# Performance work log

Measured on AMD Instinct MI355X. Metric: run time of the kernel, lower is better.

The kernel has to match this reference:

```python
import jax, jax.numpy as jnp
import numpy as np

HIDDEN = 2048
INTER = 8192
COMPRESSION = 128.9

def _n_ctrl(out_size, in_size):
    return max(16, int(out_size * in_size / COMPRESSION))

def _catmull_rom_grid(n_ctrl, n_samples):
    # static (numpy, float64) sampling grid over [0, n_ctrl-1] to avoid fp32 precision loss
    t = np.linspace(0.0, n_ctrl - 1.0, n_samples, dtype=np.float64)
    i = np.clip(np.floor(t).astype(np.int64), 0, n_ctrl - 2)
    f = (t - i).astype(np.float32)
    idx = np.stack([np.clip(i + k, 0, n_ctrl - 1) for k in (-1, 0, 1, 2)], axis=0)  # [4, N]
    return jnp.asarray(idx.astype(np.int32)), jnp.asarray(f)

def spline_reconstruct(control_points, out_size, in_size):
    """Cubic (Catmull-Rom, order-3) interpolation of 1D control points to a dense [out,in] weight."""
    n = out_size * in_size
    idx, f = _catmull_rom_grid(control_points.shape[0], n)
    p0, p1, p2, p3 = control_points[idx[0]], control_points[idx[1]], control_points[idx[2]], control_points[idx[3]]
    f2 = f * f
    f3 = f2 * f
    w = 0.5 * (2.0 * p1 + (p2 - p0) * f
               + (2.0 * p0 - 5.0 * p1 + 4.0 * p2 - p3) * f2
               + (3.0 * p1 - p0 - 3.0 * p2 + p3) * f3)
    return w.reshape(out_size, in_size)

def setup_inputs() -> dict:
    key = jax.random.key(0)
    k0, k1, k2, k3 = jax.random.split(key, 4)
    hidden_states = jax.random.normal(k0, (4, 2048, HIDDEN), dtype=jnp.float32)
    gate_cp = jax.random.normal(k1, (_n_ctrl(INTER, HIDDEN),), dtype=jnp.float32) * 0.02
    up_cp = jax.random.normal(k2, (_n_ctrl(INTER, HIDDEN),), dtype=jnp.float32) * 0.02
    down_cp = jax.random.normal(k3, (_n_ctrl(HIDDEN, INTER),), dtype=jnp.float32) * 0.02
    return {"hidden_states": hidden_states, "gate_cp": gate_cp, "up_cp": up_cp, "down_cp": down_cp}

def reference(hidden_states, gate_cp, up_cp, down_cp):
    gate_w = spline_reconstruct(gate_cp, INTER, HIDDEN)   # [I, H]
    up_w = spline_reconstruct(up_cp, INTER, HIDDEN)       # [I, H]
    down_w = spline_reconstruct(down_cp, HIDDEN, INTER)   # [H, I]
    gate = jnp.einsum('bsh,ih->bsi', hidden_states, gate_w)
    up = jnp.einsum('bsh,ih->bsi', hidden_states, up_w)
    inter = jax.nn.silu(gate) * up
    return jnp.einsum('bsi,hi->bsh', inter, down_w)
```

## Files before the change

### kernel.cpp

```cpp
#include <hip/hip_runtime.h>
#include <hip/hip_bf16.h>
#include <math.h>

using bf16 = __hip_bfloat16;
typedef __bf16 bf16x8 __attribute__((ext_vector_type(8)));
typedef float  f32x4  __attribute__((ext_vector_type(4)));

#define BK 64

__global__ void spline_recon8_kernel(const float* __restrict__ cp,
                                     bf16* __restrict__ w,
                                     int n8, int n_ctrl, double step) {
    int k8 = blockIdx.x * blockDim.x + threadIdx.x;
    if (k8 >= n8) return;
    long long kbase = (long long)k8 * 8;
    bf16x8 o;
#pragma unroll
    for (int u = 0; u < 8; ++u) {
        double t = (double)(kbase + u) * step;
        int i = (int)t;
        if (i > n_ctrl - 2) i = n_ctrl - 2;
        float f = (float)(t - (double)i);
        float p0 = cp[i > 0 ? i - 1 : 0];
        float p1 = cp[i];
        float p2 = cp[i + 1];
        float p3 = cp[(i + 2) <= (n_ctrl - 1) ? (i + 2) : (n_ctrl - 1)];
        float f2 = f * f;
        float f3 = f2 * f;
        float v = 0.5f * (2.0f * p1
                          + (p2 - p0) * f
                          + (2.0f * p0 - 5.0f * p1 + 4.0f * p2 - p3) * f2
                          + (3.0f * p1 - p0 - 3.0f * p2 + p3) * f3);
        o[u] = (__bf16)v;
    }
    *reinterpret_cast<bf16x8*>(w + kbase) = o;
}

__global__ void cvt_f32_bf16_8_kernel(const float4* __restrict__ x,
                                      bf16* __restrict__ y, int n8) {
    int k = blockIdx.x * blockDim.x + threadIdx.x;
    if (k >= n8) return;
    float4 a = x[2 * k];
    float4 b = x[2 * k + 1];
    bf16x8 o;
    o[0] = (__bf16)a.x; o[1] = (__bf16)a.y; o[2] = (__bf16)a.z; o[3] = (__bf16)a.w;
    o[4] = (__bf16)b.x; o[5] = (__bf16)b.y; o[6] = (__bf16)b.z; o[7] = (__bf16)b.w;
    *reinterpret_cast<bf16x8*>(y + (long long)k * 8) = o;
}

__device__ __forceinline__ void async_load16(const bf16* g, bf16* l) {
    __builtin_amdgcn_global_load_lds(
        (const __attribute__((address_space(1))) void*)g,
        (__attribute__((address_space(3))) void*)l,
        16, 0, 0);
}

__global__ __launch_bounds__(512, 4) void fused_gate_up_kernel(
    const bf16* __restrict__ A,
    const bf16* __restrict__ Bg,
    const bf16* __restrict__ Bu,
    bf16* __restrict__ C,
    int M, int N, int K) {
    __shared__ __align__(16) bf16 smem[3 * 128 * BK];
    bf16* As  = smem;
    bf16* Bgs = smem + 128 * BK;
    bf16* Bus = smem + 2 * 128 * BK;

    const int tid  = threadIdx.x;
    const int lane = tid & 63;
    const int wave = tid >> 6;
    const int wq   = wave & 3;
    const int wm   = (wq >> 1) * 64;
    const int wn   = (wq & 1) * 64;
    const bool is_gate = wave < 4;

    const long long brow = (long long)blockIdx.y * 128;
    const long long bcol = (long long)blockIdx.x * 128;

    const int srow = tid >> 3;
    const int skb  = ((tid & 7) ^ (srow & 7)) * 8;
    const bf16* ga0 = A  + (brow + srow) * (long long)K + skb;
    const bf16* ga1 = A  + (brow + srow + 64) * (long long)K + skb;
    const bf16* gg0 = Bg + (bcol + srow) * (long long)K + skb;
    const bf16* gg1 = Bg + (bcol + srow + 64) * (long long)K + skb;
    const bf16* gu0 = Bu + (bcol + srow) * (long long)K + skb;
    const bf16* gu1 = Bu + (bcol + srow + 64) * (long long)K + skb;
    bf16* la0 = As  + tid * 8;
    bf16* la1 = As  + 4096 + tid * 8;
    bf16* lg0 = Bgs + tid * 8;
    bf16* lg1 = Bgs + 4096 + tid * 8;
    bf16* lu0 = Bus + tid * 8;
    bf16* lu1 = Bus + 4096 + tid * 8;

    const bf16* Bsel = is_gate ? Bgs : Bus;
    const int fm = wm + (lane & 15);
    const int fn = wn + (lane & 15);
    const int qk = lane >> 4;

    f32x4 acc[4][4] = {};

    for (int k0 = 0; k0 < K; k0 += BK) {
        async_load16(ga0, la0); ga0 += BK;
        async_load16(ga1, la1); ga1 += BK;
        async_load16(gg0, lg0); gg0 += BK;
        async_load16(gg1, lg1); gg1 += BK;
        async_load16(gu0, lu0); gu0 += BK;
        async_load16(gu1, lu1); gu1 += BK;
        __syncthreads();

#pragma unroll
        for (int h = 0; h < 2; ++h) {
            bf16x8 afr[4], bfr[4];
            const int hc = (h << 2) | qk;
            const int ccA = (hc ^ (fm & 7)) * 8;
            const int ccB = (hc ^ (fn & 7)) * 8;
#pragma unroll
            for (int i = 0; i < 4; ++i)
                afr[i] = *reinterpret_cast<const bf16x8*>(
                    &As[(fm + i * 16) * BK + ccA]);
#pragma unroll
            for (int j = 0; j < 4; ++j)
                bfr[j] = *reinterpret_cast<const bf16x8*>(
                    &Bsel[(fn + j * 16) * BK + ccB]);
#pragma unroll
            for (int i = 0; i < 4; ++i)
#pragma unroll
                for (int j = 0; j < 4; ++j)
                    acc[i][j] = __builtin_amdgcn_mfma_f32_16x16x32_bf16(
                        afr[i], bfr[j], acc[i][j], 0, 0, 0);
        }
        __syncthreads();
    }

    bf16* Epi = smem;
    if (is_gate) {
#pragma unroll
        for (int i = 0; i < 4; ++i)
#pragma unroll
            for (int j = 0; j < 4; ++j)
#pragma unroll
                for (int r = 0; r < 4; ++r) {
                    int row = wm + i * 16 + (lane >> 4) * 4 + r;
                    int col = wn + j * 16 + (lane & 15);
                    float v = acc[i][j][r];
                    float s = v / (1.0f + expf(-v));
                    Epi[row * 128 + col] = __float2bfloat16(s);
                }
    }
    __syncthreads();
    if (!is_gate) {
#pragma unroll
        for (int i = 0; i < 4; ++i)
#pragma unroll
            for (int j = 0; j < 4; ++j)
#pragma unroll
                for (int r = 0; r < 4; ++r) {
                    int row = wm + i * 16 + (lane >> 4) * 4 + r;
                    int col = wn + j * 16 + (lane & 15);
                    float s = __bfloat162float(Epi[row * 128 + col]);
                    float v = s * acc[i][j][r];
                    C[(brow + row) * (long long)N + bcol + col] = __float2bfloat16(v);
                }
    }
}

__global__ __launch_bounds__(256, 4) void gemm_down3_kernel(
    const bf16* __restrict__ A,
    const bf16* __restrict__ B,
    float* __restrict__ C,
    int M, int N, int K) {
    __shared__ __align__(16) bf16 As[128 * BK];
    __shared__ __align__(16) bf16 Bs[128 * BK];

    const int tid  = threadIdx.x;
    const int lane = tid & 63;
    const int wave = tid >> 6;
    const int wm   = (wave >> 1) * 64;
    const int wn   = (wave & 1) * 64;

    const long long brow = (long long)blockIdx.y * 128;
    const long long bcol = (long long)blockIdx.x * 128;

    const int srow = tid >> 3;
    const int skb  = ((tid & 7) ^ (srow & 7)) * 8;
    const bf16* ga = A + (brow + srow) * (long long)K + skb;
    const bf16* gb = B + (bcol + srow) * (long long)K + skb;
    const long long rstep = 32LL * K;

    const int fm = wm + (lane & 15);
    const int fn = wn + (lane & 15);
    const int qk = lane >> 4;

    f32x4 acc[4][4] = {};

    for (int k0 = 0; k0 < K; k0 += BK) {
#pragma unroll
        for (int r = 0; r < 4; ++r) {
            async_load16(ga + r * rstep, As + r * 2048 + tid * 8);
            async_load16(gb + r * rstep, Bs + r * 2048 + tid * 8);
        }
        ga += BK; gb += BK;
        __syncthreads();

#pragma unroll
        for (int h = 0; h < 2; ++h) {
            bf16x8 afr[4], bfr[4];
            const int hc = (h << 2) | qk;
            const int ccA = (hc ^ (fm & 7)) * 8;
            const int ccB = (hc ^ (fn & 7)) * 8;
#pragma unroll
            for (int i = 0; i < 4; ++i)
                afr[i] = *reinterpret_cast<const bf16x8*>(
                    &As[(fm + i * 16) * BK + ccA]);
#pragma unroll
            for (int j = 0; j < 4; ++j)
                bfr[j] = *reinterpret_cast<const bf16x8*>(
                    &Bs[(fn + j * 16) * BK + ccB]);
#pragma unroll
            for (int i = 0; i < 4; ++i)
#pragma unroll
                for (int j = 0; j < 4; ++j)
                    acc[i][j] = __builtin_amdgcn_mfma_f32_16x16x32_bf16(
                        afr[i], bfr[j], acc[i][j], 0, 0, 0);
        }
        __syncthreads();
    }

#pragma unroll
    for (int i = 0; i < 4; ++i)
#pragma unroll
        for (int j = 0; j < 4; ++j)
#pragma unroll
            for (int r = 0; r < 4; ++r) {
                long long row = brow + wm + i * 16 + qk * 4 + r;
                long long col = bcol + wn + j * 16 + (lane & 15);
                C[row * N + col] = acc[i][j][r];
            }
}

extern "C" void kernel_launch(void* const* d_in, const int* in_sizes, int n_in,
                              void* d_out, int out_size, void* d_ws, size_t ws_size,
                              hipStream_t stream) {
    const float* hs  = (const float*)d_in[0];
    const float* gcp = (const float*)d_in[1];
    const float* ucp = (const float*)d_in[2];
    const float* dcp = (const float*)d_in[3];

    const int M = 8192;
    const int H = 2048;
    const int I = 8192;
    const int NW = H * I;
    const int n_ctrl_g = in_sizes[1];
    const int n_ctrl_u = in_sizes[2];
    const int n_ctrl_d = in_sizes[3];

    bf16* Xb    = (bf16*)d_ws;
    bf16* Wg    = Xb + (size_t)M * H;
    bf16* Wu    = Wg + (size_t)NW;
    bf16* Wd    = Wu + (size_t)NW;
    bf16* inter = Wd + (size_t)NW;

    const int nX8 = (M * H) / 8;
    cvt_f32_bf16_8_kernel<<<(nX8 + 255) / 256, 256, 0, stream>>>(
        (const float4*)hs, Xb, nX8);

    double step_g = (double)(n_ctrl_g - 1) / (double)(NW - 1);
    double step_u = (double)(n_ctrl_u - 1) / (double)(NW - 1);
    double step_d = (double)(n_ctrl_d - 1) / (double)(NW - 1);
    const int n8 = NW / 8;
    spline_recon8_kernel<<<(n8 + 255) / 256, 256, 0, stream>>>(gcp, Wg, n8, n_ctrl_g, step_g);
    spline_recon8_kernel<<<(n8 + 255) / 256, 256, 0, stream>>>(ucp, Wu, n8, n_ctrl_u, step_u);
    spline_recon8_kernel<<<(n8 + 255) / 256, 256, 0, stream>>>(dcp, Wd, n8, n_ctrl_d, step_d);

    fused_gate_up_kernel<<<dim3(I / 128, M / 128), 512, 0, stream>>>(
        Xb, Wg, Wu, inter, M, I, H);

    gemm_down3_kernel<<<dim3(H / 128, M / 128), 256, 0, stream>>>(
        inter, Wd, (float*)d_out, M, H, I);
}
```

Before: 924.7 us.

## Widen down-projection GEMM tile to 128x256 with 8 waves per block

The down-projection GEMM now uses 512-thread blocks, each covering a 128x256 output tile with 8 waves in a 2x4 grid, in place of 256-thread blocks over 128x128 tiles. Each A tile is loaded once per block and reused across twice as many output columns, cutting global and L2 traffic for the intermediate activations. In exchange the grid has half as many blocks (8x64=512), shared memory per block grows, and occupancy may fall on a machine with many CUs.

Measured after the change: 898.5 us. 1.03x faster.

```diff
diff --git a/kernel.cpp b/kernel.cpp
--- a/kernel.cpp
+++ b/kernel.cpp
@@ -164,28 +164,38 @@
     }
 }
 
-__global__ __launch_bounds__(256, 4) void gemm_down3_kernel(
+__global__ __launch_bounds__(512, 4) void gemm_down4_kernel(
     const bf16* __restrict__ A,
     const bf16* __restrict__ B,
     float* __restrict__ C,
     int M, int N, int K) {
-    __shared__ __align__(16) bf16 As[128 * BK];
-    __shared__ __align__(16) bf16 Bs[128 * BK];
+    __shared__ __align__(16) bf16 smem[3 * 128 * BK];
+    bf16* As = smem;
+    bf16* Bs = smem + 128 * BK;
 
     const int tid  = threadIdx.x;
     const int lane = tid & 63;
     const int wave = tid >> 6;
-    const int wm   = (wave >> 1) * 64;
-    const int wn   = (wave & 1) * 64;
+    const int wm   = (wave >> 2) * 64;
+    const int wn   = (wave & 3) * 64;
 
     const long long brow = (long long)blockIdx.y * 128;
-    const long long bcol = (long long)blockIdx.x * 128;
+    const long long bcol = (long long)blockIdx.x * 256;
 
     const int srow = tid >> 3;
     const int skb  = ((tid & 7) ^ (srow & 7)) * 8;
-    const bf16* ga = A + (brow + srow) * (long long)K + skb;
-    const bf16* gb = B + (bcol + srow) * (long long)K + skb;
-    const long long rstep = 32LL * K;
+    const bf16* ga0 = A + (brow + srow) * (long long)K + skb;
+    const bf16* ga1 = A + (brow + srow + 64) * (long long)K + skb;
+    const bf16* gb0 = B + (bcol + srow) * (long long)K + skb;
+    const bf16* gb1 = B + (bcol + srow + 64) * (long long)K + skb;
+    const bf16* gb2 = B + (bcol + srow + 128) * (long long)K + skb;
+    const bf16* gb3 = B + (bcol + srow + 192) * (long long)K + skb;
+    bf16* la0 = As + tid * 8;
+    bf16* la1 = As + 4096 + tid * 8;
+    bf16* lb0 = Bs + tid * 8;
+    bf16* lb1 = Bs + 4096 + tid * 8;
+    bf16* lb2 = Bs + 8192 + tid * 8;
+    bf16* lb3 = Bs + 12288 + tid * 8;
 
     const int fm = wm + (lane & 15);
     const int fn = wn + (lane & 15);
@@ -194,12 +204,12 @@
     f32x4 acc[4][4] = {};
 
     for (int k0 = 0; k0 < K; k0 += BK) {
-#pragma unroll
-        for (int r = 0; r < 4; ++r) {
-            async_load16(ga + r * rstep, As + r * 2048 + tid * 8);
-            async_load16(gb + r * rstep, Bs + r * 2048 + tid * 8);
-        }
-        ga += BK; gb += BK;
+        async_load16(ga0, la0); ga0 += BK;
+        async_load16(ga1, la1); ga1 += BK;
+        async_load16(gb0, lb0); gb0 += BK;
+        async_load16(gb1, lb1); gb1 += BK;
+        async_load16(gb2, lb2); gb2 += BK;
+        async_load16(gb3, lb3); gb3 += BK;
         __syncthreads();
 
 #pragma unroll
@@ -275,6 +285,6 @@
     fused_gate_up_kernel<<<dim3(I / 128, M / 128), 512, 0, stream>>>(
         Xb, Wg, Wu, inter, M, I, H);
 
-    gemm_down3_kernel<<<dim3(H / 128, M / 128), 256, 0, stream>>>(
+    gemm_down4_kernel<<<dim3(H / 256, M / 128), 512, 0, stream>>>(
         inter, Wd, (float*)d_out, M, H, I);
 }
```
